# Optimization experiments

Hardware: AMD Instinct MI355X
Metric: run time of the kernel (lower is better)

## Reference

```python
import jax, jax.numpy as jnp
import numpy as np

N, E = 100000, 1600000
F_IN, H, HG, L, C = 128, 128, 128, 3, 40


def setup_inputs() -> dict:
    key = jax.random.key(0)
    ks = jax.random.split(key, 12)
    s = 0.05
    return dict(
        x=jax.random.normal(ks[0], (N, F_IN), jnp.float32),
        edge_index=jax.random.randint(ks[1], (2, E), 0, N),
        edge_weight=jax.random.uniform(ks[2], (E,), jnp.float32),
        h0=jax.random.normal(ks[3], (N, HG), jnp.float32),
        linW=jax.random.normal(ks[4], (F_IN, H), jnp.float32) * s,
        linB=jnp.zeros((H,), jnp.float32),
        convW=jax.random.normal(ks[5], (L, H, H), jnp.float32) * s,
        convB=jnp.zeros((L, H), jnp.float32),
        gru_Wih=jax.random.normal(ks[6], (3 * HG, H), jnp.float32) * s,
        gru_Whh=jax.random.normal(ks[7], (3 * HG, HG), jnp.float32) * s,
        gru_bih=jnp.zeros((3 * HG,), jnp.float32),
        gru_bhh=jnp.zeros((3 * HG,), jnp.float32),
        fcW=jax.random.normal(ks[8], (HG, C), jnp.float32) * s,
        fcB=jnp.zeros((C,), jnp.float32),
    )


def _gru(x, h, Wih, Whh, bih, bhh):
    # torch.nn.GRUCell math (gate order: r, z, n)
    gi = x @ Wih.T + bih  # [N, 3*HG]
    gh = h @ Whh.T + bhh  # [N, 3*HG]
    ir, iz, in_ = jnp.split(gi, 3, axis=-1)
    hr, hz, hn = jnp.split(gh, 3, axis=-1)
    r = jax.nn.sigmoid(ir + hr)
    z = jax.nn.sigmoid(iz + hz)
    n = jnp.tanh(in_ + r * hn)
    return (1.0 - z) * n + z * h


def _gcn_conv(x, src, dst, ew, W, b, n_nodes):
    # PyG GCNConv: linear -> symmetric-normalized sparse aggregation -> bias
    xw = x @ W  # [N, H]
    deg = jax.ops.segment_sum(ew, dst, num_segments=n_nodes)
    dinv = jnp.where(deg > 0, jax.lax.rsqrt(deg), 0.0)
    norm = dinv[src] * ew * dinv[dst]  # [E+N]
    msg = xw[src] * norm[:, None]      # gather + scale (irregular access)
    out = jax.ops.segment_sum(msg, dst, num_segments=n_nodes)  # scatter-add
    return out + b


def reference(x, edge_index, edge_weight, h0, linW, linB, convW, convB,
              gru_Wih, gru_Whh, gru_bih, gru_bhh, fcW, fcB):
    n_nodes = x.shape[0]
    # GCNConv default: add self-loops with weight 1 before normalization
    loops = jnp.arange(n_nodes)
    src = jnp.concatenate([edge_index[0], loops])
    dst = jnp.concatenate([edge_index[1], loops])
    ew = jnp.concatenate([edge_weight, jnp.ones((n_nodes,), edge_weight.dtype)])

    h = h0
    xh = jax.nn.relu(x @ linW + linB)
    h = _gru(xh, h, gru_Wih, gru_Whh, gru_bih, gru_bhh)
    for l in range(convW.shape[0]):  # fixed small layer count
        xh = jax.nn.relu(_gcn_conv(xh, src, dst, ew, convW[l], convB[l], n_nodes))
        h = _gru(xh, h, gru_Wih, gru_Whh, gru_bih, gru_bhh)
    return h @ fcW + fcB
```

## Files before the change

### kernel.cpp

```cpp
#include <hip/hip_runtime.h>
#include <hip/hip_bf16.h>
#include <math.h>

typedef __attribute__((ext_vector_type(8))) short bf8_t;
typedef __attribute__((ext_vector_type(4))) float f4_t;
typedef __attribute__((ext_vector_type(8))) unsigned short us8_t;

__device__ inline unsigned short f2bf(float f) {
  union { float f; unsigned u; } x; x.f = f;
  unsigned r = x.u + 0x7FFF + ((x.u >> 16) & 1);
  return (unsigned short)(r >> 16);
}
__device__ inline float bflo(unsigned v) {
  union { unsigned u; float f; } x; x.u = v << 16; return x.f;
}
__device__ inline float bfhi(unsigned v) {
  union { unsigned u; float f; } x; x.u = v & 0xFFFF0000u; return x.f;
}
__device__ inline float fast_sig(float x) {
  return __builtin_amdgcn_rcpf(1.f + __expf(-x));
}
__device__ inline float fast_tanh(float x) {
  return 1.f - 2.f * __builtin_amdgcn_rcpf(1.f + __expf(2.f * x));
}

__device__ inline void async_copy16(const void* g, void* l) {
  __builtin_amdgcn_global_load_lds(
      (const __attribute__((address_space(1))) unsigned int*)g,
      (__attribute__((address_space(3))) unsigned int*)l, 16, 0, 0);
}


__device__ inline void packB_body(const float* __restrict__ W,
                                  unsigned short* __restrict__ out,
                                  int K, int Ncols, int ldw, int trans, int bid) {
  int idx = bid * 256 + threadIdx.x;
  int total = (Ncols / 16) * (K / 32) * 64;
  if (idx >= total) return;
  int lane = idx & 63;
  int frag = idx >> 6;
  int kt = K / 32;
  int k0 = frag % kt;
  int n0 = frag / kt;
  int n = n0 * 16 + (lane & 15);
  int kbase = k0 * 32 + (lane >> 4) * 8;
  us8_t v;
#pragma unroll
  for (int j = 0; j < 8; ++j) {
    int k = kbase + j;
    float f = trans ? W[(size_t)n * ldw + k] : W[(size_t)k * ldw + n];
    v[j] = f2bf(f);
  }
  *(us8_t*)(out + (size_t)idx * 8) = v;
}

__device__ inline void fill_body(const int* __restrict__ src, const int* __restrict__ dst,
                                 const float* __restrict__ ew, const int* __restrict__ rowptr,
                                 const int* __restrict__ pos, int2* __restrict__ csr,
                                 int E, int bid) {
  int e = bid * 512 + threadIdx.x;
  if (e >= E) return;
  int d = dst[e];
  int p = rowptr[d] + pos[e];
  unsigned long long v = (unsigned long long)(unsigned)src[e] |
                         ((unsigned long long)(unsigned)__float_as_int(ew[e]) << 32);
  __builtin_nontemporal_store(v, (unsigned long long*)(csr + p));
}

__device__ inline void deg_body(const int* __restrict__ rowptr, const int2* __restrict__ csr,
                                float* __restrict__ dinv, int N, int bid) {
  int n = bid * 512 + threadIdx.x;
  if (n >= N) return;
  int b = rowptr[n], e = rowptr[n + 1];
  float s = 1.0f;
  for (int j = b; j < e; ++j) {
    unsigned long long v = __builtin_nontemporal_load((const unsigned long long*)(csr + j));
    s += __int_as_float((int)(v >> 32));
  }
  dinv[n] = rsqrtf(s);
}

__device__ inline void norm_body(const int* __restrict__ rowptr, int2* __restrict__ csr,
                                 const float* __restrict__ dinv, int N, int bid) {
  int n = bid * 512 + threadIdx.x;
  if (n >= N) return;
  int b = rowptr[n], e = rowptr[n + 1];
  float dn = dinv[n];
  for (int j = b; j < e; ++j) {
    unsigned long long v = __builtin_nontemporal_load((const unsigned long long*)(csr + j));
    int s = (int)v;
    float w = dinv[s] * __int_as_float((int)(v >> 32)) * dn;
    unsigned long long nv = (unsigned long long)(unsigned)s |
                            ((unsigned long long)(unsigned)__float_as_int(w) << 32);
    __builtin_nontemporal_store(nv, (unsigned long long*)(csr + j));
  }
}

__device__ inline void gemm_body8(const unsigned short* __restrict__ A,
                                  const unsigned short* __restrict__ Bp,
                                  const float* __restrict__ bias,
                                  unsigned short* __restrict__ C, int M, int bid,
                                  bool relu, bool hasbias, unsigned char* smem) {
  int wave = threadIdx.x >> 6, lane = threadIdx.x & 63;
  int row0 = (bid * 8 + wave) * 16;
  int m = lane & 15, q = lane >> 4;

#pragma unroll
  for (int i = 0; i < 4; ++i) {
    int f = wave * 4 + i;
    async_copy16((const unsigned char*)Bp + (size_t)f * 1024 + lane * 16,
                 smem + f * 1024);
  }
  __syncthreads();
  if (row0 >= M) return;

  int arow = row0 + m; if (arow >= M) arow = M - 1;
  bf8_t a[4];
#pragma unroll
  for (int k0 = 0; k0 < 4; ++k0)
    a[k0] = *(const bf8_t*)(A + (size_t)arow * 128 + k0 * 32 + q * 8);

#pragma unroll
  for (int n0 = 0; n0 < 8; ++n0) {
    f4_t acc = {};
#pragma unroll
    for (int k0 = 0; k0 < 4; ++k0) {
      bf8_t b = *(const bf8_t*)(smem + (n0 * 4 + k0) * 1024 + lane * 16);
      acc = __builtin_amdgcn_mfma_f32_16x16x32_bf16(a[k0], b, acc, 0, 0, 0);
    }
    int col = n0 * 16 + m;
    float bs = hasbias ? bias[col] : 0.f;
#pragma unroll
    for (int r = 0; r < 4; ++r) {
      int grow = row0 + q * 4 + r;
      if (grow < M) {
        float v = acc[r] + bs;
        if (relu) v = fmaxf(v, 0.f);
        C[(size_t)grow * 128 + col] = f2bf(v);
      }
    }
  }
}

__device__ inline void gru_stage8(const unsigned short* __restrict__ Bi,
                                  const unsigned short* __restrict__ Bh,
                                  unsigned char* smem, int wave, int lane, int g) {
#pragma unroll
  for (int i = 0; i < 3; ++i) {
    int f = wave * 3 + i;
    int s = f >> 2, k0 = f & 3;
    int cc = g + 8 * (s >= 3 ? s - 3 : s);
    const unsigned short* src = (s < 3) ? Bi : Bh;
    async_copy16((const unsigned char*)src + ((size_t)(cc * 4 + k0)) * 1024 + lane * 16,
                 smem + f * 1024);
  }
}

__device__ inline void gru_core(const bf8_t* ax, const float* h_in, float* h_out,
                                const unsigned short* __restrict__ Bi,
                                const unsigned short* __restrict__ Bh,
                                const float* __restrict__ bih, const float* __restrict__ bhh,
                                int M, int row0, int wave, int lane, unsigned char* smem) {
  int m = lane & 15, q = lane >> 4;
  int arow = row0 + m; if (arow >= M) arow = M - 1;

  bf8_t ah[4];
#pragma unroll
  for (int k0 = 0; k0 < 4; ++k0) {
    const float* hp = h_in + (size_t)arow * 128 + k0 * 32 + q * 8;
    float4 h0 = *(const float4*)hp;
    float4 h1 = *(const float4*)(hp + 4);
    bf8_t t;
    t[0] = (short)f2bf(h0.x); t[1] = (short)f2bf(h0.y);
    t[2] = (short)f2bf(h0.z); t[3] = (short)f2bf(h0.w);
    t[4] = (short)f2bf(h1.x); t[5] = (short)f2bf(h1.y);
    t[6] = (short)f2bf(h1.z); t[7] = (short)f2bf(h1.w);
    ah[k0] = t;
  }

  for (int g = 0; g < 8; ++g) {
    __syncthreads();
    f4_t air = {}, aiz = {}, ain = {}, ahr = {}, ahz = {}, ahn = {};
#pragma unroll
    for (int k0 = 0; k0 < 4; ++k0) {
      bf8_t br = *(const bf8_t*)(smem + (0 * 4 + k0) * 1024 + lane * 16);
      bf8_t bz = *(const bf8_t*)(smem + (1 * 4 + k0) * 1024 + lane * 16);
      bf8_t bn = *(const bf8_t*)(smem + (2 * 4 + k0) * 1024 + lane * 16);
      bf8_t cr = *(const bf8_t*)(smem + (3 * 4 + k0) * 1024 + lane * 16);
      bf8_t cz = *(const bf8_t*)(smem + (4 * 4 + k0) * 1024 + lane * 16);
      bf8_t cn = *(const bf8_t*)(smem + (5 * 4 + k0) * 1024 + lane * 16);
      air = __builtin_amdgcn_mfma_f32_16x16x32_bf16(ax[k0], br, air, 0, 0, 0);
      aiz = __builtin_amdgcn_mfma_f32_16x16x32_bf16(ax[k0], bz, aiz, 0, 0, 0);
      ain = __builtin_amdgcn_mfma_f32_16x16x32_bf16(ax[k0], bn, ain, 0, 0, 0);
      ahr = __builtin_amdgcn_mfma_f32_16x16x32_bf16(ah[k0], cr, ahr, 0, 0, 0);
      ahz = __builtin_amdgcn_mfma_f32_16x16x32_bf16(ah[k0], cz, ahz, 0, 0, 0);
      ahn = __builtin_amdgcn_mfma_f32_16x16x32_bf16(ah[k0], cn, ahn, 0, 0, 0);
    }
    __syncthreads();
    if (g < 7) gru_stage8(Bi, Bh, smem, wave, lane, g + 1);

    int col = g * 16 + m;
    float bir_ = bih[col], biz_ = bih[col + 128], bin_ = bih[col + 256];
    float bhr_ = bhh[col], bhz_ = bhh[col + 128], bhn_ = bhh[col + 256];
#pragma unroll
    for (int r = 0; r < 4; ++r) {
      int grow = row0 + q * 4 + r;
      if (grow < M) {
        float hprev = h_in[(size_t)grow * 128 + col];
        float rr = fast_sig(air[r] + bir_ + ahr[r] + bhr_);
        float zz = fast_sig(aiz[r] + biz_ + ahz[r] + bhz_);
        float nn = fast_tanh(ain[r] + bin_ + rr * (ahn[r] + bhn_));
        h_out[(size_t)grow * 128 + col] = (1.f - zz) * nn + zz * hprev;
      }
    }
  }
}

__device__ inline void gru_body8(const unsigned short* __restrict__ xh,
                                 const float* h_in, float* h_out,
                                 const unsigned short* __restrict__ Bi,
                                 const unsigned short* __restrict__ Bh,
                                 const float* __restrict__ bih, const float* __restrict__ bhh,
                                 int M, int bid, unsigned char* smem) {
  int wave = threadIdx.x >> 6, lane = threadIdx.x & 63;
  int row0 = (bid * 8 + wave) * 16;
  gru_stage8(Bi, Bh, smem, wave, lane, 0);
  int m = lane & 15, q = lane >> 4;
  int arow = row0 + m; if (arow >= M) arow = M - 1;
  bf8_t ax[4];
#pragma unroll
  for (int k0 = 0; k0 < 4; ++k0)
    ax[k0] = *(const bf8_t*)(xh + (size_t)arow * 128 + k0 * 32 + q * 8);
  gru_core(ax, h_in, h_out, Bi, Bh, bih, bhh, M, row0, wave, lane, smem);
}


__global__ __launch_bounds__(256) void k_prep(
    const float* __restrict__ linW, const float* __restrict__ convW,
    const float* __restrict__ Wih, const float* __restrict__ Whh,
    unsigned short* __restrict__ linWp, unsigned short* __restrict__ convWp,
    unsigned short* __restrict__ Bi, unsigned short* __restrict__ Bh,
    int* __restrict__ cnt, int N) {
  int b = blockIdx.x;
  if (b < 8)  { packB_body(linW, linWp, 128, 128, 128, 0, b); return; }
  if (b < 32) { int l = (b - 8) >> 3;
                packB_body(convW + (size_t)l * 16384, convWp + (size_t)l * 16384,
                           128, 128, 128, 0, (b - 8) & 7); return; }
  if (b < 56) { packB_body(Wih, Bi, 128, 384, 128, 1, b - 32); return; }
  if (b < 80) { packB_body(Whh, Bh, 128, 384, 128, 1, b - 56); return; }
  int i = (b - 80) * 256 + threadIdx.x;
  if (i < N) cnt[i] = 0;
}

__global__ __launch_bounds__(256) void k_count_f2bf(
    const int* __restrict__ dst, int* __restrict__ cnt, int* __restrict__ pos, int E,
    const float* __restrict__ xin, unsigned short* __restrict__ xout, size_t n8,
    int nCnt) {
  if ((int)blockIdx.x < nCnt) {
    int e = blockIdx.x * 256 + threadIdx.x;
    if (e < E) pos[e] = atomicAdd(&cnt[dst[e]], 1);
    return;
  }
  size_t i = (size_t)(blockIdx.x - nCnt) * 256 + threadIdx.x;
  if (i >= n8) return;
  const float4* p = (const float4*)(xin + i * 8);
  float4 a = p[0], b = p[1];
  us8_t v;
  v[0] = f2bf(a.x); v[1] = f2bf(a.y); v[2] = f2bf(a.z); v[3] = f2bf(a.w);
  v[4] = f2bf(b.x); v[5] = f2bf(b.y); v[6] = f2bf(b.z); v[7] = f2bf(b.w);
  *(us8_t*)(xout + i * 8) = v;
}

__global__ __launch_bounds__(256) void k_scan_block(
    const int* __restrict__ cnt, int* __restrict__ partial,
    int* __restrict__ bsum, int n) {
  __shared__ int s[256];
  int tid = threadIdx.x;
  int i = blockIdx.x * 256 + tid;
  s[tid] = (i < n) ? cnt[i] : 0;
  __syncthreads();
#pragma unroll
  for (int d = 1; d < 256; d <<= 1) {
    int t = (tid >= d) ? s[tid - d] : 0;
    __syncthreads();
    s[tid] += t;
    __syncthreads();
  }
  if (i < n) partial[i] = s[tid];
  if (tid == 255) bsum[blockIdx.x] = s[255];
}

__global__ __launch_bounds__(512) void k_scan_sums(int* __restrict__ bsum, int nb) {
  __shared__ int s[512];
  int tid = threadIdx.x;
  s[tid] = (tid < nb) ? bsum[tid] : 0;
  __syncthreads();
#pragma unroll
  for (int d = 1; d < 512; d <<= 1) {
    int t = (tid >= d) ? s[tid - d] : 0;
    __syncthreads();
    s[tid] += t;
    __syncthreads();
  }
  if (tid < nb) bsum[tid] = s[tid];
}

__global__ __launch_bounds__(256) void k_scan_add(
    const int* __restrict__ partial, const int* __restrict__ bsum,
    int* __restrict__ rowptr, int n) {
  int i = blockIdx.x * 256 + threadIdx.x;
  if (i == 0) rowptr[0] = 0;
  if (i < n) {
    int v = partial[i] + (blockIdx.x > 0 ? bsum[blockIdx.x - 1] : 0);
    rowptr[i + 1] = v;
  }
}

__global__ __launch_bounds__(512, 4) void k_fill_lin(
    const int* __restrict__ src, const int* __restrict__ dstI,
    const float* __restrict__ ew, const int* __restrict__ rowptr,
    const int* __restrict__ pos, int2* __restrict__ csr, int E,
    const unsigned short* __restrict__ A, const unsigned short* __restrict__ Bp,
    const float* __restrict__ bias, unsigned short* __restrict__ C, int M,
    int nFill) {
  __shared__ unsigned char smem[32 * 1024];
  if ((int)blockIdx.x < nFill) {
    fill_body(src, dstI, ew, rowptr, pos, csr, E, blockIdx.x);
    return;
  }
  gemm_body8(A, Bp, bias, C, M, blockIdx.x - nFill, true, true, smem);
}

__global__ __launch_bounds__(512, 4) void k_deg_gru(
    const int* __restrict__ rowptr, const int2* __restrict__ csr,
    float* __restrict__ dinv, int N,
    const unsigned short* __restrict__ xh, const float* h_in, float* h_out,
    const unsigned short* __restrict__ Bi, const unsigned short* __restrict__ Bh,
    const float* __restrict__ bih, const float* __restrict__ bhh, int M,
    int nDeg) {
  __shared__ unsigned char smem[24 * 1024];
  if ((int)blockIdx.x < nDeg) {
    deg_body(rowptr, csr, dinv, N, blockIdx.x);
    return;
  }
  gru_body8(xh, h_in, h_out, Bi, Bh, bih, bhh, M, blockIdx.x - nDeg, smem);
}

__global__ __launch_bounds__(512, 4) void k_norm_conv(
    const int* __restrict__ rowptr, int2* __restrict__ csr,
    const float* __restrict__ dinv, int N,
    const unsigned short* __restrict__ A, const unsigned short* __restrict__ Bp,
    unsigned short* __restrict__ C, int M, int nNorm) {
  __shared__ unsigned char smem[32 * 1024];
  if ((int)blockIdx.x < nNorm) {
    norm_body(rowptr, csr, dinv, N, blockIdx.x);
    return;
  }
  gemm_body8(A, Bp, nullptr, C, M, blockIdx.x - nNorm, false, false, smem);
}

__global__ __launch_bounds__(512, 4) void k_gru_conv(
    const unsigned short* __restrict__ xh, const float* h_in, float* h_out,
    const unsigned short* __restrict__ Bi, const unsigned short* __restrict__ Bh,
    const float* __restrict__ bih, const float* __restrict__ bhh,
    const unsigned short* __restrict__ Bp, unsigned short* __restrict__ xw,
    int M, int nGru) {
  __shared__ unsigned char smem[32 * 1024];
  if ((int)blockIdx.x < nGru) {
    gru_body8(xh, h_in, h_out, Bi, Bh, bih, bhh, M, blockIdx.x, smem);
    return;
  }
  gemm_body8(xh, Bp, nullptr, xw, M, blockIdx.x - nGru, false, false, smem);
}

__global__ __launch_bounds__(512, 4) void k_gru(
    const unsigned short* __restrict__ xh, const float* h_in, float* h_out,
    const unsigned short* __restrict__ Bi, const unsigned short* __restrict__ Bh,
    const float* __restrict__ bih, const float* __restrict__ bhh, int M) {
  __shared__ unsigned char smem[24 * 1024];
  gru_body8(xh, h_in, h_out, Bi, Bh, bih, bhh, M, blockIdx.x, smem);
}


__global__ __launch_bounds__(256) void k_gather(
    const int* __restrict__ rowptr, const int2* __restrict__ csr,
    const unsigned* __restrict__ xw,
    const float* __restrict__ dinv, const float* __restrict__ bias,
    unsigned* __restrict__ out, int N) {
  int wave = threadIdx.x >> 6;
  int lane = threadIdx.x & 63;
  int node = __builtin_amdgcn_readfirstlane(blockIdx.x * 4 + wave);
  if (node >= N) return;
  int beg = __builtin_amdgcn_readfirstlane(rowptr[node]);
  int end = __builtin_amdgcn_readfirstlane(rowptr[node + 1]);

  float accl = 0.f, acch = 0.f;
  int k = beg;
  for (; k + 4 <= end; k += 4) {
    unsigned long long r0 = __builtin_nontemporal_load((const unsigned long long*)(csr + k));
    unsigned long long r1 = __builtin_nontemporal_load((const unsigned long long*)(csr + k + 1));
    unsigned long long r2 = __builtin_nontemporal_load((const unsigned long long*)(csr + k + 2));
    unsigned long long r3 = __builtin_nontemporal_load((const unsigned long long*)(csr + k + 3));
    unsigned v0 = xw[((size_t)(unsigned)r0 << 6) + lane];
    unsigned v1 = xw[((size_t)(unsigned)r1 << 6) + lane];
    unsigned v2 = xw[((size_t)(unsigned)r2 << 6) + lane];
    unsigned v3 = xw[((size_t)(unsigned)r3 << 6) + lane];
    float w0 = __int_as_float((int)(r0 >> 32)), w1 = __int_as_float((int)(r1 >> 32));
    float w2 = __int_as_float((int)(r2 >> 32)), w3 = __int_as_float((int)(r3 >> 32));
    accl += bflo(v0) * w0; acch += bfhi(v0) * w0;
    accl += bflo(v1) * w1; acch += bfhi(v1) * w1;
    accl += bflo(v2) * w2; acch += bfhi(v2) * w2;
    accl += bflo(v3) * w3; acch += bfhi(v3) * w3;
  }
  for (; k < end; ++k) {
    unsigned long long r = __builtin_nontemporal_load((const unsigned long long*)(csr + k));
    unsigned v = xw[((size_t)(unsigned)r << 6) + lane];
    float w = __int_as_float((int)(r >> 32));
    accl += bflo(v) * w; acch += bfhi(v) * w;
  }

  float di = dinv[node];
  float sn = di * di;
  unsigned vs = xw[((size_t)node << 6) + lane];
  float2 b = *(const float2*)(bias + lane * 2);
  float rl = fmaxf(accl + bflo(vs) * sn + b.x, 0.f);
  float rh = fmaxf(acch + bfhi(vs) * sn + b.y, 0.f);
  unsigned o = (unsigned)f2bf(rl) | ((unsigned)f2bf(rh) << 16);
  out[((size_t)node << 6) + lane] = o;
}


template<bool RELU, bool BIAS>
__global__ __launch_bounds__(256) void k_gemm128(
    const float* __restrict__ A, const float* __restrict__ B,
    const float* __restrict__ bias, float* __restrict__ C, int M, int Nc) {
  __shared__ float As[64][36];
  __shared__ float Bs[32][64];
  int tid = threadIdx.x;
  int tx = tid & 15, ty = tid >> 4;
  int row0 = blockIdx.y * 64, col0 = blockIdx.x * 64;
  float acc[4][4] = {};

  for (int k0 = 0; k0 < 128; k0 += 32) {
#pragma unroll
    for (int i = 0; i < 2; ++i) {
      int f = tid + i * 256;
      int r = f >> 3, c4 = f & 7;
      int gr = row0 + r;
      float4 v = make_float4(0.f, 0.f, 0.f, 0.f);
      if (gr < M) v = *(const float4*)(A + (size_t)gr * 128 + k0 + c4 * 4);
      *(float4*)(&As[r][c4 * 4]) = v;
    }
#pragma unroll
    for (int i = 0; i < 2; ++i) {
      int f = tid + i * 256;
      int r = f >> 4, c4 = f & 15;
      int gc = col0 + c4 * 4;
      float4 v = make_float4(0.f, 0.f, 0.f, 0.f);
      if (gc + 3 < Nc) v = *(const float4*)(B + (size_t)(k0 + r) * Nc + gc);
      *(float4*)(&Bs[r][c4 * 4]) = v;
    }
    __syncthreads();
#pragma unroll
    for (int kk = 0; kk < 32; ++kk) {
      float4 b = *(float4*)(&Bs[kk][tx * 4]);
      float a0 = As[ty * 4 + 0][kk];
      float a1 = As[ty * 4 + 1][kk];
      float a2 = As[ty * 4 + 2][kk];
      float a3 = As[ty * 4 + 3][kk];
      acc[0][0] += a0 * b.x; acc[0][1] += a0 * b.y; acc[0][2] += a0 * b.z; acc[0][3] += a0 * b.w;
      acc[1][0] += a1 * b.x; acc[1][1] += a1 * b.y; acc[1][2] += a1 * b.z; acc[1][3] += a1 * b.w;
      acc[2][0] += a2 * b.x; acc[2][1] += a2 * b.y; acc[2][2] += a2 * b.z; acc[2][3] += a2 * b.w;
      acc[3][0] += a3 * b.x; acc[3][1] += a3 * b.y; acc[3][2] += a3 * b.z; acc[3][3] += a3 * b.w;
    }
    __syncthreads();
  }

#pragma unroll
  for (int i = 0; i < 4; ++i) {
    int gr = row0 + ty * 4 + i;
    if (gr >= M) continue;
#pragma unroll
    for (int j = 0; j < 4; ++j) {
      int gc = col0 + tx * 4 + j;
      if (gc >= Nc) continue;
      float v = acc[i][j];
      if (BIAS) v += bias[gc];
      if (RELU) v = fmaxf(v, 0.f);
      C[(size_t)gr * Nc + gc] = v;
    }
  }
}


extern "C" void kernel_launch(void* const* d_in, const int* in_sizes, int n_in,
                              void* d_out, int out_size, void* d_ws, size_t ws_size,
                              hipStream_t stream) {
  const float* x    = (const float*)d_in[0];
  const int*   ei   = (const int*)d_in[1];
  const float* ew   = (const float*)d_in[2];
  const float* h0   = (const float*)d_in[3];
  const float* linW = (const float*)d_in[4];
  const float* linB = (const float*)d_in[5];
  const float* convW= (const float*)d_in[6];
  const float* convB= (const float*)d_in[7];
  const float* Wih  = (const float*)d_in[8];
  const float* Whh  = (const float*)d_in[9];
  const float* bih  = (const float*)d_in[10];
  const float* bhh  = (const float*)d_in[11];
  const float* fcW  = (const float*)d_in[12];
  const float* fcB  = (const float*)d_in[13];

  int N = in_sizes[0] / 128;
  int E = in_sizes[1] / 2;
  const int* srcI = ei;
  const int* dstI = ei + E;
  int nb = (N + 255) / 256;

  float* ws = (float*)d_ws;
  size_t off = 0;
  float* dinv = ws + off; off += (size_t)N;
  if (off & 1) off++;
  float* h    = ws + off; off += (size_t)N * 128;
  int* iws = (int*)(ws + off);
  size_t ioff = 0;
  int2* csr    = (int2*)iws; ioff += (size_t)2 * E;
  int* cnt     = iws + ioff; ioff += (size_t)N;
  int* partial = iws + ioff; ioff += (size_t)N;
  int* bsum    = iws + ioff; ioff += 512;
  int* rowptr  = iws + ioff; ioff += (size_t)N + 1;
  ioff = (ioff + 3) & ~(size_t)3;
  unsigned short* usws = (unsigned short*)(iws + ioff);
  size_t uoff = 0;
  unsigned short* x_bf   = usws + uoff; uoff += (size_t)N * 128;
  unsigned short* xh_bf  = usws + uoff; uoff += (size_t)N * 128;
  unsigned short* xw_bf  = usws + uoff; uoff += (size_t)N * 128;
  unsigned short* linWp  = usws + uoff; uoff += 128 * 128;
  unsigned short* convWp = usws + uoff; uoff += 3 * 128 * 128;
  unsigned short* Bi     = usws + uoff; uoff += 384 * 128;
  unsigned short* Bh     = usws + uoff; uoff += 384 * 128;

  int* pos = (int*)xw_bf;

  int gw8  = (N + 127) / 128;
  int nCnt = (E + 255) / 256;
  int nF2  = (int)(((size_t)N * 16 + 255) / 256);
  int n512 = (N + 511) / 512;
  int e512 = (E + 511) / 512;

  k_prep<<<80 + nb, 256, 0, stream>>>(linW, convW, Wih, Whh,
                                      linWp, convWp, Bi, Bh, cnt, N);
  k_count_f2bf<<<nCnt + nF2, 256, 0, stream>>>(dstI, cnt, pos, E,
                                               x, x_bf, (size_t)N * 16, nCnt);
  k_scan_block<<<nb, 256, 0, stream>>>(cnt, partial, bsum, N);
  k_scan_sums<<<1, 512, 0, stream>>>(bsum, nb);
  k_scan_add<<<nb, 256, 0, stream>>>(partial, bsum, rowptr, N);
  k_fill_lin<<<e512 + gw8, 512, 0, stream>>>(srcI, dstI, ew, rowptr, pos, csr, E,
                                             x_bf, linWp, linB, xh_bf, N, e512);
  k_deg_gru<<<n512 + gw8, 512, 0, stream>>>(rowptr, csr, dinv, N,
                                            xh_bf, h0, h, Bi, Bh, bih, bhh, N, n512);
  k_norm_conv<<<n512 + gw8, 512, 0, stream>>>(rowptr, csr, dinv, N,
                                              xh_bf, convWp, xw_bf, N, n512);

  int ggat = (N + 3) / 4;
  k_gather<<<ggat, 256, 0, stream>>>(rowptr, csr, (const unsigned*)xw_bf, dinv,
                                     convB, (unsigned*)xh_bf, N);
  k_gru_conv<<<2 * gw8, 512, 0, stream>>>(
      xh_bf, h, h, Bi, Bh, bih, bhh,
      convWp + (size_t)1 * 128 * 128, xw_bf, N, gw8);
  k_gather<<<ggat, 256, 0, stream>>>(rowptr, csr, (const unsigned*)xw_bf, dinv,
                                     convB + 128, (unsigned*)xh_bf, N);
  k_gru_conv<<<2 * gw8, 512, 0, stream>>>(
      xh_bf, h, h, Bi, Bh, bih, bhh,
      convWp + (size_t)2 * 128 * 128, xw_bf, N, gw8);
  k_gather<<<ggat, 256, 0, stream>>>(rowptr, csr, (const unsigned*)xw_bf, dinv,
                                     convB + 256, (unsigned*)xh_bf, N);
  k_gru<<<gw8, 512, 0, stream>>>(xh_bf, h, h, Bi, Bh, bih, bhh, N);
  dim3 g40(1, (N + 63) / 64);
  k_gemm128<false, true><<<g40, 256, 0, stream>>>(h, fcW, fcB, (float*)d_out, N, 40);
}
```

Before: 969.7 us.

## Co-schedule GRU with sparse gather using ping-pong xh buffers; prefetch hprev

Restructures the launch schedule so each GRU step runs in the same kernel as the next layer's sparse gather. Two xh buffers are alternated so the gather can write new features while the GRU reads the previous ones. The conv GEMM moves into its own kernel, and degree computation is paired with the first conv GEMM, with norm as a separate launch. Inside the GRU core, the previous-h values for the next column group are prefetched into registers during the MFMA loop, instead of being loaded in the epilogue. This adds register pressure and mixes heterogeneous block types, which can hurt occupancy balance.

```diff
diff --git a/kernel.cpp b/kernel.cpp
--- a/kernel.cpp
+++ b/kernel.cpp
@@ -178,6 +178,19 @@
     ah[k0] = t;
   }
 
+  int erow[4];
+#pragma unroll
+  for (int r = 0; r < 4; ++r) {
+    int gr = row0 + q * 4 + r;
+    erow[r] = (gr < M) ? gr : (M - 1);
+  }
+
+  float hp_cur[4], hp_nxt[4];
+#pragma unroll
+  for (int r = 0; r < 4; ++r)
+    hp_cur[r] = h_in[(size_t)erow[r] * 128 + m];
+
+#pragma unroll
   for (int g = 0; g < 8; ++g) {
     __syncthreads();
     f4_t air = {}, aiz = {}, ain = {}, ahr = {}, ahz = {}, ahn = {};
@@ -196,6 +209,11 @@
       ahz = __builtin_amdgcn_mfma_f32_16x16x32_bf16(ah[k0], cz, ahz, 0, 0, 0);
       ahn = __builtin_amdgcn_mfma_f32_16x16x32_bf16(ah[k0], cn, ahn, 0, 0, 0);
     }
+    if (g < 7) {
+#pragma unroll
+      for (int r = 0; r < 4; ++r)
+        hp_nxt[r] = h_in[(size_t)erow[r] * 128 + (g + 1) * 16 + m];
+    }
     __syncthreads();
     if (g < 7) gru_stage8(Bi, Bh, smem, wave, lane, g + 1);
 
@@ -206,13 +224,14 @@
     for (int r = 0; r < 4; ++r) {
       int grow = row0 + q * 4 + r;
       if (grow < M) {
-        float hprev = h_in[(size_t)grow * 128 + col];
         float rr = fast_sig(air[r] + bir_ + ahr[r] + bhr_);
         float zz = fast_sig(aiz[r] + biz_ + ahz[r] + bhz_);
         float nn = fast_tanh(ain[r] + bin_ + rr * (ahn[r] + bhn_));
-        h_out[(size_t)grow * 128 + col] = (1.f - zz) * nn + zz * hprev;
+        h_out[(size_t)grow * 128 + col] = (1.f - zz) * nn + zz * hp_cur[r];
       }
     }
+#pragma unroll
+    for (int r = 0; r < 4; ++r) hp_cur[r] = hp_nxt[r];
   }
 }
 
@@ -234,162 +253,14 @@
   gru_core(ax, h_in, h_out, Bi, Bh, bih, bhh, M, row0, wave, lane, smem);
 }
 
-
-__global__ __launch_bounds__(256) void k_prep(
-    const float* __restrict__ linW, const float* __restrict__ convW,
-    const float* __restrict__ Wih, const float* __restrict__ Whh,
-    unsigned short* __restrict__ linWp, unsigned short* __restrict__ convWp,
-    unsigned short* __restrict__ Bi, unsigned short* __restrict__ Bh,
-    int* __restrict__ cnt, int N) {
-  int b = blockIdx.x;
-  if (b < 8)  { packB_body(linW, linWp, 128, 128, 128, 0, b); return; }
-  if (b < 32) { int l = (b - 8) >> 3;
-                packB_body(convW + (size_t)l * 16384, convWp + (size_t)l * 16384,
-                           128, 128, 128, 0, (b - 8) & 7); return; }
-  if (b < 56) { packB_body(Wih, Bi, 128, 384, 128, 1, b - 32); return; }
-  if (b < 80) { packB_body(Whh, Bh, 128, 384, 128, 1, b - 56); return; }
-  int i = (b - 80) * 256 + threadIdx.x;
-  if (i < N) cnt[i] = 0;
-}
-
-__global__ __launch_bounds__(256) void k_count_f2bf(
-    const int* __restrict__ dst, int* __restrict__ cnt, int* __restrict__ pos, int E,
-    const float* __restrict__ xin, unsigned short* __restrict__ xout, size_t n8,
-    int nCnt) {
-  if ((int)blockIdx.x < nCnt) {
-    int e = blockIdx.x * 256 + threadIdx.x;
-    if (e < E) pos[e] = atomicAdd(&cnt[dst[e]], 1);
-    return;
-  }
-  size_t i = (size_t)(blockIdx.x - nCnt) * 256 + threadIdx.x;
-  if (i >= n8) return;
-  const float4* p = (const float4*)(xin + i * 8);
-  float4 a = p[0], b = p[1];
-  us8_t v;
-  v[0] = f2bf(a.x); v[1] = f2bf(a.y); v[2] = f2bf(a.z); v[3] = f2bf(a.w);
-  v[4] = f2bf(b.x); v[5] = f2bf(b.y); v[6] = f2bf(b.z); v[7] = f2bf(b.w);
-  *(us8_t*)(xout + i * 8) = v;
-}
-
-__global__ __launch_bounds__(256) void k_scan_block(
-    const int* __restrict__ cnt, int* __restrict__ partial,
-    int* __restrict__ bsum, int n) {
-  __shared__ int s[256];
-  int tid = threadIdx.x;
-  int i = blockIdx.x * 256 + tid;
-  s[tid] = (i < n) ? cnt[i] : 0;
-  __syncthreads();
-#pragma unroll
-  for (int d = 1; d < 256; d <<= 1) {
-    int t = (tid >= d) ? s[tid - d] : 0;
-    __syncthreads();
-    s[tid] += t;
-    __syncthreads();
-  }
-  if (i < n) partial[i] = s[tid];
-  if (tid == 255) bsum[blockIdx.x] = s[255];
-}
-
-__global__ __launch_bounds__(512) void k_scan_sums(int* __restrict__ bsum, int nb) {
-  __shared__ int s[512];
-  int tid = threadIdx.x;
-  s[tid] = (tid < nb) ? bsum[tid] : 0;
-  __syncthreads();
-#pragma unroll
-  for (int d = 1; d < 512; d <<= 1) {
-    int t = (tid >= d) ? s[tid - d] : 0;
-    __syncthreads();
-    s[tid] += t;
-    __syncthreads();
-  }
-  if (tid < nb) bsum[tid] = s[tid];
-}
-
-__global__ __launch_bounds__(256) void k_scan_add(
-    const int* __restrict__ partial, const int* __restrict__ bsum,
-    int* __restrict__ rowptr, int n) {
-  int i = blockIdx.x * 256 + threadIdx.x;
-  if (i == 0) rowptr[0] = 0;
-  if (i < n) {
-    int v = partial[i] + (blockIdx.x > 0 ? bsum[blockIdx.x - 1] : 0);
-    rowptr[i + 1] = v;
-  }
-}
-
-__global__ __launch_bounds__(512, 4) void k_fill_lin(
-    const int* __restrict__ src, const int* __restrict__ dstI,
-    const float* __restrict__ ew, const int* __restrict__ rowptr,
-    const int* __restrict__ pos, int2* __restrict__ csr, int E,
-    const unsigned short* __restrict__ A, const unsigned short* __restrict__ Bp,
-    const float* __restrict__ bias, unsigned short* __restrict__ C, int M,
-    int nFill) {
-  __shared__ unsigned char smem[32 * 1024];
-  if ((int)blockIdx.x < nFill) {
-    fill_body(src, dstI, ew, rowptr, pos, csr, E, blockIdx.x);
-    return;
-  }
-  gemm_body8(A, Bp, bias, C, M, blockIdx.x - nFill, true, true, smem);
-}
-
-__global__ __launch_bounds__(512, 4) void k_deg_gru(
+__device__ inline void gather_body(
     const int* __restrict__ rowptr, const int2* __restrict__ csr,
-    float* __restrict__ dinv, int N,
-    const unsigned short* __restrict__ xh, const float* h_in, float* h_out,
-    const unsigned short* __restrict__ Bi, const unsigned short* __restrict__ Bh,
-    const float* __restrict__ bih, const float* __restrict__ bhh, int M,
-    int nDeg) {
-  __shared__ unsigned char smem[24 * 1024];
-  if ((int)blockIdx.x < nDeg) {
-    deg_body(rowptr, csr, dinv, N, blockIdx.x);
-    return;
-  }
-  gru_body8(xh, h_in, h_out, Bi, Bh, bih, bhh, M, blockIdx.x - nDeg, smem);
-}
-
-__global__ __launch_bounds__(512, 4) void k_norm_conv(
-    const int* __restrict__ rowptr, int2* __restrict__ csr,
-    const float* __restrict__ dinv, int N,
-    const unsigned short* __restrict__ A, const unsigned short* __restrict__ Bp,
-    unsigned short* __restrict__ C, int M, int nNorm) {
-  __shared__ unsigned char smem[32 * 1024];
-  if ((int)blockIdx.x < nNorm) {
-    norm_body(rowptr, csr, dinv, N, blockIdx.x);
-    return;
-  }
-  gemm_body8(A, Bp, nullptr, C, M, blockIdx.x - nNorm, false, false, smem);
-}
-
-__global__ __launch_bounds__(512, 4) void k_gru_conv(
-    const unsigned short* __restrict__ xh, const float* h_in, float* h_out,
-    const unsigned short* __restrict__ Bi, const unsigned short* __restrict__ Bh,
-    const float* __restrict__ bih, const float* __restrict__ bhh,
-    const unsigned short* __restrict__ Bp, unsigned short* __restrict__ xw,
-    int M, int nGru) {
-  __shared__ unsigned char smem[32 * 1024];
-  if ((int)blockIdx.x < nGru) {
-    gru_body8(xh, h_in, h_out, Bi, Bh, bih, bhh, M, blockIdx.x, smem);
-    return;
-  }
-  gemm_body8(xh, Bp, nullptr, xw, M, blockIdx.x - nGru, false, false, smem);
-}
-
-__global__ __launch_bounds__(512, 4) void k_gru(
-    const unsigned short* __restrict__ xh, const float* h_in, float* h_out,
-    const unsigned short* __restrict__ Bi, const unsigned short* __restrict__ Bh,
-    const float* __restrict__ bih, const float* __restrict__ bhh, int M) {
-  __shared__ unsigned char smem[24 * 1024];
-  gru_body8(xh, h_in, h_out, Bi, Bh, bih, bhh, M, blockIdx.x, smem);
-}
-
-
-__global__ __launch_bounds__(256) void k_gather(
-    const int* __restrict__ rowptr, const int2* __restrict__ csr,
-    const unsigned* __restrict__ xw,
-    const float* __restrict__ dinv, const float* __restrict__ bias,
-    unsigned* __restrict__ out, int N) {
+    const unsigned* __restrict__ xw, const float* __restrict__ dinv,
+    const float* __restrict__ bias, unsigned* __restrict__ out,
+    int N, int nodeBase) {
   int wave = threadIdx.x >> 6;
   int lane = threadIdx.x & 63;
-  int node = __builtin_amdgcn_readfirstlane(blockIdx.x * 4 + wave);
+  int node = __builtin_amdgcn_readfirstlane(nodeBase + wave);
   if (node >= N) return;
   int beg = __builtin_amdgcn_readfirstlane(rowptr[node]);
   int end = __builtin_amdgcn_readfirstlane(rowptr[node + 1]);
@@ -427,6 +298,152 @@
   float rh = fmaxf(acch + bfhi(vs) * sn + b.y, 0.f);
   unsigned o = (unsigned)f2bf(rl) | ((unsigned)f2bf(rh) << 16);
   out[((size_t)node << 6) + lane] = o;
+}
+
+
+__global__ __launch_bounds__(256) void k_prep(
+    const float* __restrict__ linW, const float* __restrict__ convW,
+    const float* __restrict__ Wih, const float* __restrict__ Whh,
+    unsigned short* __restrict__ linWp, unsigned short* __restrict__ convWp,
+    unsigned short* __restrict__ Bi, unsigned short* __restrict__ Bh,
+    int* __restrict__ cnt, int N) {
+  int b = blockIdx.x;
+  if (b < 8)  { packB_body(linW, linWp, 128, 128, 128, 0, b); return; }
+  if (b < 32) { int l = (b - 8) >> 3;
+                packB_body(convW + (size_t)l * 16384, convWp + (size_t)l * 16384,
+                           128, 128, 128, 0, (b - 8) & 7); return; }
+  if (b < 56) { packB_body(Wih, Bi, 128, 384, 128, 1, b - 32); return; }
+  if (b < 80) { packB_body(Whh, Bh, 128, 384, 128, 1, b - 56); return; }
+  int i = (b - 80) * 256 + threadIdx.x;
+  if (i < N) cnt[i] = 0;
+}
+
+__global__ __launch_bounds__(256) void k_count_f2bf(
+    const int* __restrict__ dst, int* __restrict__ cnt, int* __restrict__ pos, int E,
+    const float* __restrict__ xin, unsigned short* __restrict__ xout, size_t n8,
+    int nCnt) {
+  if ((int)blockIdx.x < nCnt) {
+    int e = blockIdx.x * 256 + threadIdx.x;
+    if (e < E) pos[e] = atomicAdd(&cnt[dst[e]], 1);
+    return;
+  }
+  size_t i = (size_t)(blockIdx.x - nCnt) * 256 + threadIdx.x;
+  if (i >= n8) return;
+  const float4* p = (const float4*)(xin + i * 8);
+  float4 a = p[0], b = p[1];
+  us8_t v;
+  v[0] = f2bf(a.x); v[1] = f2bf(a.y); v[2] = f2bf(a.z); v[3] = f2bf(a.w);
+  v[4] = f2bf(b.x); v[5] = f2bf(b.y); v[6] = f2bf(b.z); v[7] = f2bf(b.w);
+  *(us8_t*)(xout + i * 8) = v;
+}
+
+__global__ __launch_bounds__(256) void k_scan_block(
+    const int* __restrict__ cnt, int* __restrict__ partial,
+    int* __restrict__ bsum, int n) {
+  __shared__ int s[256];
+  int tid = threadIdx.x;
+  int i = blockIdx.x * 256 + tid;
+  s[tid] = (i < n) ? cnt[i] : 0;
+  __syncthreads();
+#pragma unroll
+  for (int d = 1; d < 256; d <<= 1) {
+    int t = (tid >= d) ? s[tid - d] : 0;
+    __syncthreads();
+    s[tid] += t;
+    __syncthreads();
+  }
+  if (i < n) partial[i] = s[tid];
+  if (tid == 255) bsum[blockIdx.x] = s[255];
+}
+
+__global__ __launch_bounds__(512) void k_scan_sums(int* __restrict__ bsum, int nb) {
+  __shared__ int s[512];
+  int tid = threadIdx.x;
+  s[tid] = (tid < nb) ? bsum[tid] : 0;
+  __syncthreads();
+#pragma unroll
+  for (int d = 1; d < 512; d <<= 1) {
+    int t = (tid >= d) ? s[tid - d] : 0;
+    __syncthreads();
+    s[tid] += t;
+    __syncthreads();
+  }
+  if (tid < nb) bsum[tid] = s[tid];
+}
+
+__global__ __launch_bounds__(256) void k_scan_add(
+    const int* __restrict__ partial, const int* __restrict__ bsum,
+    int* __restrict__ rowptr, int n) {
+  int i = blockIdx.x * 256 + threadIdx.x;
+  if (i == 0) rowptr[0] = 0;
+  if (i < n) {
+    int v = partial[i] + (blockIdx.x > 0 ? bsum[blockIdx.x - 1] : 0);
+    rowptr[i + 1] = v;
+  }
+}
+
+__global__ __launch_bounds__(512, 4) void k_fill_lin(
+    const int* __restrict__ src, const int* __restrict__ dstI,
+    const float* __restrict__ ew, const int* __restrict__ rowptr,
+    const int* __restrict__ pos, int2* __restrict__ csr, int E,
+    const unsigned short* __restrict__ A, const unsigned short* __restrict__ Bp,
+    const float* __restrict__ bias, unsigned short* __restrict__ C, int M,
+    int nFill) {
+  __shared__ unsigned char smem[32 * 1024];
+  if ((int)blockIdx.x < nFill) {
+    fill_body(src, dstI, ew, rowptr, pos, csr, E, blockIdx.x);
+    return;
+  }
+  gemm_body8(A, Bp, bias, C, M, blockIdx.x - nFill, true, true, smem);
+}
+
+__global__ __launch_bounds__(512, 4) void k_deg_conv(
+    const int* __restrict__ rowptr, const int2* __restrict__ csr,
+    float* __restrict__ dinv, int N,
+    const unsigned short* __restrict__ A, const unsigned short* __restrict__ Bp,
+    unsigned short* __restrict__ C, int M, int nDeg) {
+  __shared__ unsigned char smem[32 * 1024];
+  if ((int)blockIdx.x < nDeg) {
+    deg_body(rowptr, csr, dinv, N, blockIdx.x);
+    return;
+  }
+  gemm_body8(A, Bp, nullptr, C, M, blockIdx.x - nDeg, false, false, smem);
+}
+
+__global__ __launch_bounds__(512) void k_norm(
+    const int* __restrict__ rowptr, int2* __restrict__ csr,
+    const float* __restrict__ dinv, int N) {
+  norm_body(rowptr, csr, dinv, N, blockIdx.x);
+}
+
+__global__ __launch_bounds__(512, 4) void k_gather_gru(
+    const int* __restrict__ rowptr, const int2* __restrict__ csr,
+    const unsigned* __restrict__ xw, const float* __restrict__ dinv,
+    const float* __restrict__ bias, unsigned* __restrict__ xh_out, int N,
+    const unsigned short* __restrict__ xh_gru, const float* h_in, float* h_out,
+    const unsigned short* __restrict__ Bi, const unsigned short* __restrict__ Bh,
+    const float* __restrict__ bih, const float* __restrict__ bhh, int nGru) {
+  __shared__ unsigned char smem[24 * 1024];
+  if ((int)blockIdx.x < nGru) {
+    gru_body8(xh_gru, h_in, h_out, Bi, Bh, bih, bhh, N, blockIdx.x, smem);
+    return;
+  }
+  gather_body(rowptr, csr, xw, dinv, bias, xh_out, N, (blockIdx.x - nGru) * 8);
+}
+
+__global__ __launch_bounds__(512, 4) void k_conv(
+    const unsigned short* __restrict__ A, const unsigned short* __restrict__ Bp,
+    unsigned short* __restrict__ C, int M) {
+  __shared__ unsigned char smem[32 * 1024];
+  gemm_body8(A, Bp, nullptr, C, M, blockIdx.x, false, false, smem);
+}
+
+__global__ __launch_bounds__(512, 4) void k_gru(
+    const unsigned short* __restrict__ xh, const float* h_in, float* h_out,
+    const unsigned short* __restrict__ Bi, const unsigned short* __restrict__ Bh,
+    const float* __restrict__ bih, const float* __restrict__ bhh, int M) {
+  __shared__ unsigned char smem[24 * 1024];
+  gru_body8(xh, h_in, h_out, Bi, Bh, bih, bhh, M, blockIdx.x, smem);
 }
 
 
@@ -541,12 +558,15 @@
   unsigned short* Bh     = usws + uoff; uoff += 384 * 128;
 
   int* pos = (int*)xw_bf;
-
-  int gw8  = (N + 127) / 128;
-  int nCnt = (E + 255) / 256;
-  int nF2  = (int)(((size_t)N * 16 + 255) / 256);
-  int n512 = (N + 511) / 512;
-  int e512 = (E + 511) / 512;
+  unsigned short* xhA = xh_bf;
+  unsigned short* xhB = x_bf;
+
+  int gw8   = (N + 127) / 128;
+  int nCnt  = (E + 255) / 256;
+  int nF2   = (int)(((size_t)N * 16 + 255) / 256);
+  int n512  = (N + 511) / 512;
+  int e512  = (E + 511) / 512;
+  int nGat8 = (N + 7) / 8;
 
   k_prep<<<80 + nb, 256, 0, stream>>>(linW, convW, Wih, Whh,
                                       linWp, convWp, Bi, Bh, cnt, N);
@@ -556,26 +576,22 @@
   k_scan_sums<<<1, 512, 0, stream>>>(bsum, nb);
   k_scan_add<<<nb, 256, 0, stream>>>(partial, bsum, rowptr, N);
   k_fill_lin<<<e512 + gw8, 512, 0, stream>>>(srcI, dstI, ew, rowptr, pos, csr, E,
-                                             x_bf, linWp, linB, xh_bf, N, e512);
-  k_deg_gru<<<n512 + gw8, 512, 0, stream>>>(rowptr, csr, dinv, N,
-                                            xh_bf, h0, h, Bi, Bh, bih, bhh, N, n512);
-  k_norm_conv<<<n512 + gw8, 512, 0, stream>>>(rowptr, csr, dinv, N,
-                                              xh_bf, convWp, xw_bf, N, n512);
-
-  int ggat = (N + 3) / 4;
-  k_gather<<<ggat, 256, 0, stream>>>(rowptr, csr, (const unsigned*)xw_bf, dinv,
-                                     convB, (unsigned*)xh_bf, N);
-  k_gru_conv<<<2 * gw8, 512, 0, stream>>>(
-      xh_bf, h, h, Bi, Bh, bih, bhh,
-      convWp + (size_t)1 * 128 * 128, xw_bf, N, gw8);
-  k_gather<<<ggat, 256, 0, stream>>>(rowptr, csr, (const unsigned*)xw_bf, dinv,
-                                     convB + 128, (unsigned*)xh_bf, N);
-  k_gru_conv<<<2 * gw8, 512, 0, stream>>>(
-      xh_bf, h, h, Bi, Bh, bih, bhh,
-      convWp + (size_t)2 * 128 * 128, xw_bf, N, gw8);
-  k_gather<<<ggat, 256, 0, stream>>>(rowptr, csr, (const unsigned*)xw_bf, dinv,
-                                     convB + 256, (unsigned*)xh_bf, N);
-  k_gru<<<gw8, 512, 0, stream>>>(xh_bf, h, h, Bi, Bh, bih, bhh, N);
+                                             x_bf, linWp, linB, xhA, N, e512);
+  k_deg_conv<<<n512 + gw8, 512, 0, stream>>>(rowptr, csr, dinv, N,
+                                             xhA, convWp, xw_bf, N, n512);
+  k_norm<<<n512, 512, 0, stream>>>(rowptr, csr, dinv, N);
+  k_gather_gru<<<gw8 + nGat8, 512, 0, stream>>>(
+      rowptr, csr, (const unsigned*)xw_bf, dinv, convB, (unsigned*)xhB, N,
+      xhA, h0, h, Bi, Bh, bih, bhh, gw8);
+  k_conv<<<gw8, 512, 0, stream>>>(xhB, convWp + (size_t)1 * 128 * 128, xw_bf, N);
+  k_gather_gru<<<gw8 + nGat8, 512, 0, stream>>>(
+      rowptr, csr, (const unsigned*)xw_bf, dinv, convB + 128, (unsigned*)xhA, N,
+      xhB, h, h, Bi, Bh, bih, bhh, gw8);
+  k_conv<<<gw8, 512, 0, stream>>>(xhA, convWp + (size_t)2 * 128 * 128, xw_bf, N);
+  k_gather_gru<<<gw8 + nGat8, 512, 0, stream>>>(
+      rowptr, csr, (const unsigned*)xw_bf, dinv, convB + 256, (unsigned*)xhB, N,
+      xhA, h, h, Bi, Bh, bih, bhh, gw8);
+  k_gru<<<gw8, 512, 0, stream>>>(xhB, h, h, Bi, Bh, bih, bhh, N);
   dim3 g40(1, (N + 63) / 64);
   k_gemm128<false, true><<<g40, 256, 0, stream>>>(h, fcW, fcB, (float*)d_out, N, 40);
 }
```

Result: slower. 1.181 ms (+21.8%).
